# Optimization experiments

Hardware: AMD Instinct MI355X
Metric: run time of the kernel (lower is better)

## Reference

```python
import jax, jax.numpy as jnp
import numpy as np

N_NODES = 100000
N_EDGES = 1600000
D_IN = 128
D_OUT = 5


def setup_inputs() -> dict:
    key = jax.random.key(0)
    k1, k2, k3, k4, k5 = jax.random.split(key, 5)
    x = jax.random.normal(k1, (N_NODES, D_IN), dtype=jnp.float32)
    edge_index = jax.random.randint(k2, (2, N_EDGES), 0, N_NODES, dtype=jnp.int64)
    scale = 1.0 / np.sqrt(D_IN)
    W_l = jax.random.normal(k3, (D_OUT, D_IN), dtype=jnp.float32) * scale
    b_l = jax.random.normal(k4, (D_OUT,), dtype=jnp.float32) * scale
    W_r = jax.random.normal(k5, (D_OUT, D_IN), dtype=jnp.float32) * scale
    return {"x": x, "edge_index": edge_index, "W_l": W_l, "b_l": b_l, "W_r": W_r}


def reference(x, edge_index, W_l, b_l, W_r):
    # PyG SAGEConv with aggr='mean', root_weight=True:
    # out_i = mean_{j: (j->i) in E} x_j @ W_l^T + b_l + x_i @ W_r^T
    n = x.shape[0]
    src = edge_index[0]
    dst = edge_index[1]
    msgs = x[src]  # [E, D_in] gather (irregular access)
    agg_sum = jax.ops.segment_sum(msgs, dst, num_segments=n)  # [N, D_in]
    deg = jax.ops.segment_sum(jnp.ones(src.shape, dtype=x.dtype), dst, num_segments=n)
    agg_mean = agg_sum / jnp.maximum(deg, 1.0)[:, None]  # zero-degree nodes -> 0
    out = agg_mean @ W_l.T + b_l + x @ W_r.T  # [N, D_out]
    return out
```

## Files before the change

kernel.cpp:

```cpp
#include <hip/hip_runtime.h>
#include <hip/hip_bf16.h>


#define N_NODES 100000
#define N_EDGES 1600000
#define D_IN 128

#define HL_STRIDE 8
#define N_PAD 100352

#define B_NODES 196
#define N_BUCKETS 512
#define CAP 3840

#define SC_EPB 16384
#define SC_GRID ((N_EDGES + SC_EPB - 1) / SC_EPB)
#define SC_CHUNKS (SC_EPB / 1024)

#define NPG 8
#define PROJ_NPB (16 * NPG)
#define PROJ_BLOCKS ((N_NODES + PROJ_NPB - 1) / PROJ_NPB)
#define FUSED_GRID (SC_GRID + PROJ_BLOCKS)

#define FXS 262144.0f
#define FXB 16777216u
#define FXBF 16777216.0f
#define INV_FXS (1.0f / 262144.0f)

typedef unsigned long long u64;
typedef unsigned int u32;

__global__ __launch_bounds__(256, 4) void proj_scatter_kernel(
    const float* __restrict__ x,
    const float* __restrict__ Wl,
    const float* __restrict__ Wr,
    float* __restrict__ hl,
    float* __restrict__ hr,
    const int* __restrict__ ei,
    u32* __restrict__ sorted,
    int* __restrict__ cursor)
{
    const int tid = threadIdx.x;

    if (blockIdx.x < SC_GRID) {
        __shared__ int hist[N_BUCKETS];
        __shared__ int basepos[N_BUCKETS];

        for (int i = tid; i < N_BUCKETS; i += 256) hist[i] = 0;
        __syncthreads();

        const int e0 = blockIdx.x * SC_EPB;

#pragma unroll
        for (int c = 0; c < SC_CHUNKS; ++c) {
            int e = e0 + (c << 10) + (tid << 2);
            if (e < N_EDGES) {
                int4 d4 = *(const int4*)(ei + N_EDGES + e);
                atomicAdd(&hist[(unsigned)d4.x / 196u], 1);
                atomicAdd(&hist[(unsigned)d4.y / 196u], 1);
                atomicAdd(&hist[(unsigned)d4.z / 196u], 1);
                atomicAdd(&hist[(unsigned)d4.w / 196u], 1);
            }
        }
        __syncthreads();

        for (int b = tid; b < N_BUCKETS; b += 256) {
            int c = hist[b];
            if (c > 0) basepos[b] = atomicAdd(&cursor[b], c);
        }
        __syncthreads();

        for (int i = tid; i < N_BUCKETS; i += 256) hist[i] = 0;
        __syncthreads();

#pragma unroll
        for (int c = 0; c < SC_CHUNKS; ++c) {
            int e = e0 + (c << 10) + (tid << 2);
            if (e < N_EDGES) {
                int4 s4 = *(const int4*)(ei + e);
                int4 d4 = *(const int4*)(ei + N_EDGES + e);
                int sv[4] = { s4.x, s4.y, s4.z, s4.w };
                int dv[4] = { d4.x, d4.y, d4.z, d4.w };
#pragma unroll
                for (int q = 0; q < 4; ++q) {
                    unsigned b = (unsigned)dv[q] / 196u;
                    unsigned r = (unsigned)dv[q] - b * 196u;
                    int slot = atomicAdd(&hist[b], 1);
                    sorted[(size_t)b * CAP + basepos[b] + slot] =
                        (r << 17) | (unsigned)sv[q];
                }
            }
        }
    } else {
        const int pblk = blockIdx.x - SC_GRID;
        const int g = tid >> 4;
        const int k = tid & 15;

        float4 wv[10][2];
#pragma unroll
        for (int o = 0; o < 10; ++o) {
            const float* w = (o < 5 ? Wl + o * D_IN : Wr + (o - 5) * D_IN) + k * 8;
            wv[o][0] = ((const float4*)w)[0];
            wv[o][1] = ((const float4*)w)[1];
        }

        const int node0 = pblk * PROJ_NPB + g * NPG;

#pragma unroll
        for (int it = 0; it < NPG; ++it) {
            const int node = min(node0 + it, N_NODES - 1);

            const float4* xr = (const float4*)(x + (size_t)node * D_IN + k * 8);
            float4 x0 = xr[0];
            float4 x1 = xr[1];

            float s[10];
#pragma unroll
            for (int o = 0; o < 10; ++o) {
                s[o] = x0.x * wv[o][0].x + x0.y * wv[o][0].y
                     + x0.z * wv[o][0].z + x0.w * wv[o][0].w
                     + x1.x * wv[o][1].x + x1.y * wv[o][1].y
                     + x1.z * wv[o][1].z + x1.w * wv[o][1].w;
            }

#pragma unroll
            for (int o = 0; o < 10; ++o) {
                s[o] += __shfl_xor(s[o], 8, 64);
                s[o] += __shfl_xor(s[o], 4, 64);
                s[o] += __shfl_xor(s[o], 2, 64);
                s[o] += __shfl_xor(s[o], 1, 64);
            }

            if (k == 0) {
                float* pl = hl + (size_t)node * HL_STRIDE;
                *(float4*)pl = make_float4(s[0], s[1], s[2], s[3]);
                pl[4] = s[4];
                float* pr = hr + (size_t)node * HL_STRIDE;
                *(float4*)pr = make_float4(s[5], s[6], s[7], s[8]);
                pr[4] = s[9];
            }
        }
    }
}

__global__ __launch_bounds__(512) void agg_kernel(
    const u32* __restrict__ sorted,
    const int* __restrict__ cursor,
    const float* __restrict__ hl,
    const float* __restrict__ hr,
    const float* __restrict__ bias,
    float* __restrict__ out)
{
    __shared__ u64 acc[B_NODES * 3];

    const int b   = blockIdx.x;
    const int tid = threadIdx.x;

    for (int i = tid; i < B_NODES * 3; i += 512) acc[i] = 0ull;
    __syncthreads();

    const int cnt = cursor[b];
    const u32* sp = sorted + (size_t)b * CAP;
    const int nvec = cnt >> 2;

#define EMIT(hh, ee, rr)                                                     \
    {                                                                        \
        u32 f0 = __float2uint_rn(fmaf((hh).x, FXS, FXBF));                   \
        u32 f1 = __float2uint_rn(fmaf((hh).y, FXS, FXBF));                   \
        u32 f2 = __float2uint_rn(fmaf((hh).z, FXS, FXBF));                   \
        u32 f3 = __float2uint_rn(fmaf((hh).w, FXS, FXBF));                   \
        u32 f4 = __float2uint_rn(fmaf((ee),   FXS, FXBF));                   \
        u64* a = acc + (rr) * 3;                                             \
        atomicAdd(&a[0], ((u64)f1 << 32) | f0);                              \
        atomicAdd(&a[1], ((u64)f3 << 32) | f2);                              \
        atomicAdd(&a[2], ((u64)f4 << 32) | 1u);                              \
    }

    for (int it = tid; it < nvec; it += 512) {
        uint4 v = ((const uint4*)sp)[it];
        int s0 = (int)(v.x & 0x1FFFFu), r0 = (int)(v.x >> 17);
        int s1 = (int)(v.y & 0x1FFFFu), r1 = (int)(v.y >> 17);
        int s2 = (int)(v.z & 0x1FFFFu), r2 = (int)(v.z >> 17);
        int s3 = (int)(v.w & 0x1FFFFu), r3 = (int)(v.w >> 17);

        const float* p0 = hl + (size_t)s0 * HL_STRIDE;
        const float* p1 = hl + (size_t)s1 * HL_STRIDE;
        const float* p2 = hl + (size_t)s2 * HL_STRIDE;
        const float* p3 = hl + (size_t)s3 * HL_STRIDE;
        float4 h0 = *(const float4*)p0; float e0 = p0[4];
        float4 h1 = *(const float4*)p1; float e1 = p1[4];
        float4 h2 = *(const float4*)p2; float e2 = p2[4];
        float4 h3 = *(const float4*)p3; float e3 = p3[4];

        EMIT(h0, e0, r0) EMIT(h1, e1, r1) EMIT(h2, e2, r2) EMIT(h3, e3, r3)
    }
    for (int i = (nvec << 2) + tid; i < cnt; i += 512) {
        u32 v = sp[i];
        int src = (int)(v & 0x1FFFFu);
        int r   = (int)(v >> 17);
        const float* p = hl + (size_t)src * HL_STRIDE;
        float4 h = *(const float4*)p;
        float  e = p[4];
        EMIT(h, e, r)
    }
#undef EMIT
    __syncthreads();

    const int nodebase = b * B_NODES;
    for (int n = tid; n < B_NODES; n += 512) {
        int node = nodebase + n;
        if (node >= N_NODES) continue;
        u64 w0 = acc[n * 3 + 0];
        u64 w1 = acc[n * 3 + 1];
        u64 w2 = acc[n * 3 + 2];
        u32 deg = (u32)(w2 & 0xFFFFFFFFu);
        u32 db  = deg * FXB;
        int i0 = (int)((u32)(w0 & 0xFFFFFFFFu) - db);
        int i1 = (int)((u32)(w0 >> 32)         - db);
        int i2 = (int)((u32)(w1 & 0xFFFFFFFFu) - db);
        int i3 = (int)((u32)(w1 >> 32)         - db);
        int i4 = (int)((u32)(w2 >> 32)         - db);

        float rec = INV_FXS / fmaxf((float)deg, 1.0f);
        const float* h = hr + (size_t)node * HL_STRIDE;
        float* o = out + (size_t)node * 5;
        o[0] = (float)i0 * rec + bias[0] + h[0];
        o[1] = (float)i1 * rec + bias[1] + h[1];
        o[2] = (float)i2 * rec + bias[2] + h[2];
        o[3] = (float)i3 * rec + bias[3] + h[3];
        o[4] = (float)i4 * rec + bias[4] + h[4];
    }
}

extern "C" void kernel_launch(void* const* d_in, const int* in_sizes, int n_in,
                              void* d_out, int out_size, void* d_ws, size_t ws_size,
                              hipStream_t stream) {
    const float* x    = (const float*)d_in[0];
    const int*   ei   = (const int*)d_in[1];
    const float* Wl   = (const float*)d_in[2];
    const float* bl   = (const float*)d_in[3];
    const float* Wr   = (const float*)d_in[4];
    float*       out  = (float*)d_out;

    float* hl     = (float*)d_ws;
    float* hr     = hl + (size_t)N_PAD * HL_STRIDE;
    u32*   sorted = (u32*)(hr + (size_t)N_PAD * HL_STRIDE);
    int*   cursor = (int*)(sorted + (size_t)N_BUCKETS * CAP);

    hipMemsetAsync(cursor, 0, N_BUCKETS * sizeof(int), stream);

    proj_scatter_kernel<<<FUSED_GRID, 256, 0, stream>>>(
        x, Wl, Wr, hl, hr, ei, sorted, cursor);

    agg_kernel<<<N_BUCKETS, 512, 0, stream>>>(sorted, cursor, hl, hr, bl, out);
}
```

Baseline: 140.3 us.

## Keep edges in registers across scatter passes and widen aggregation gather to eight

Result: no change. 140.0 us (-0.2%).

```diff
diff --git a/kernel.cpp b/kernel.cpp
--- a/kernel.cpp
+++ b/kernel.cpp
@@ -13,9 +13,9 @@
 #define N_BUCKETS 512
 #define CAP 3840
 
-#define SC_EPB 16384
+#define SC_EPB 4096
 #define SC_GRID ((N_EDGES + SC_EPB - 1) / SC_EPB)
-#define SC_CHUNKS (SC_EPB / 1024)
+#define SC_EPT 16
 
 #define NPG 8
 #define PROJ_NPB (16 * NPG)
@@ -49,17 +49,31 @@
         for (int i = tid; i < N_BUCKETS; i += 256) hist[i] = 0;
         __syncthreads();
 
-        const int e0 = blockIdx.x * SC_EPB;
-
-#pragma unroll
-        for (int c = 0; c < SC_CHUNKS; ++c) {
-            int e = e0 + (c << 10) + (tid << 2);
-            if (e < N_EDGES) {
+        const int eb = blockIdx.x * SC_EPB;
+
+        int sv[SC_EPT], dv[SC_EPT], slot[SC_EPT];
+        bool vld[4];
+
+#pragma unroll
+        for (int c = 0; c < 4; ++c) {
+            int e = eb + (c << 10) + (tid << 2);
+            vld[c] = (e < N_EDGES);
+            if (vld[c]) {
+                int4 s4 = *(const int4*)(ei + e);
                 int4 d4 = *(const int4*)(ei + N_EDGES + e);
-                atomicAdd(&hist[(unsigned)d4.x / 196u], 1);
-                atomicAdd(&hist[(unsigned)d4.y / 196u], 1);
-                atomicAdd(&hist[(unsigned)d4.z / 196u], 1);
-                atomicAdd(&hist[(unsigned)d4.w / 196u], 1);
+                sv[c*4+0]=s4.x; sv[c*4+1]=s4.y; sv[c*4+2]=s4.z; sv[c*4+3]=s4.w;
+                dv[c*4+0]=d4.x; dv[c*4+1]=d4.y; dv[c*4+2]=d4.z; dv[c*4+3]=d4.w;
+            }
+        }
+
+#pragma unroll
+        for (int c = 0; c < 4; ++c) {
+            if (vld[c]) {
+#pragma unroll
+                for (int q = 0; q < 4; ++q) {
+                    unsigned b = (unsigned)dv[c*4+q] / 196u;
+                    slot[c*4+q] = atomicAdd(&hist[b], 1);
+                }
             }
         }
         __syncthreads();
@@ -70,24 +84,15 @@
         }
         __syncthreads();
 
-        for (int i = tid; i < N_BUCKETS; i += 256) hist[i] = 0;
-        __syncthreads();
-
-#pragma unroll
-        for (int c = 0; c < SC_CHUNKS; ++c) {
-            int e = e0 + (c << 10) + (tid << 2);
-            if (e < N_EDGES) {
-                int4 s4 = *(const int4*)(ei + e);
-                int4 d4 = *(const int4*)(ei + N_EDGES + e);
-                int sv[4] = { s4.x, s4.y, s4.z, s4.w };
-                int dv[4] = { d4.x, d4.y, d4.z, d4.w };
+#pragma unroll
+        for (int c = 0; c < 4; ++c) {
+            if (vld[c]) {
 #pragma unroll
                 for (int q = 0; q < 4; ++q) {
-                    unsigned b = (unsigned)dv[q] / 196u;
-                    unsigned r = (unsigned)dv[q] - b * 196u;
-                    int slot = atomicAdd(&hist[b], 1);
-                    sorted[(size_t)b * CAP + basepos[b] + slot] =
-                        (r << 17) | (unsigned)sv[q];
+                    unsigned b = (unsigned)dv[c*4+q] / 196u;
+                    unsigned r = (unsigned)dv[c*4+q] - b * 196u;
+                    sorted[(size_t)b * CAP + basepos[b] + slot[c*4+q]] =
+                        (r << 17) | (unsigned)sv[c*4+q];
                 }
             }
         }
@@ -161,7 +166,6 @@
 
     const int cnt = cursor[b];
     const u32* sp = sorted + (size_t)b * CAP;
-    const int nvec = cnt >> 2;
 
 #define EMIT(hh, ee, rr)                                                     \
     {                                                                        \
@@ -176,32 +180,33 @@
         atomicAdd(&a[2], ((u64)f4 << 32) | 1u);                              \
     }
 
-    for (int it = tid; it < nvec; it += 512) {
-        uint4 v = ((const uint4*)sp)[it];
-        int s0 = (int)(v.x & 0x1FFFFu), r0 = (int)(v.x >> 17);
-        int s1 = (int)(v.y & 0x1FFFFu), r1 = (int)(v.y >> 17);
-        int s2 = (int)(v.z & 0x1FFFFu), r2 = (int)(v.z >> 17);
-        int s3 = (int)(v.w & 0x1FFFFu), r3 = (int)(v.w >> 17);
-
-        const float* p0 = hl + (size_t)s0 * HL_STRIDE;
-        const float* p1 = hl + (size_t)s1 * HL_STRIDE;
-        const float* p2 = hl + (size_t)s2 * HL_STRIDE;
-        const float* p3 = hl + (size_t)s3 * HL_STRIDE;
-        float4 h0 = *(const float4*)p0; float e0 = p0[4];
-        float4 h1 = *(const float4*)p1; float e1 = p1[4];
-        float4 h2 = *(const float4*)p2; float e2 = p2[4];
-        float4 h3 = *(const float4*)p3; float e3 = p3[4];
-
-        EMIT(h0, e0, r0) EMIT(h1, e1, r1) EMIT(h2, e2, r2) EMIT(h3, e3, r3)
-    }
-    for (int i = (nvec << 2) + tid; i < cnt; i += 512) {
+    const int noct = cnt >> 3;
+    for (int it = tid; it < noct; it += 512) {
+        const uint4* sp4 = (const uint4*)sp;
+        uint4 va = sp4[it * 2];
+        uint4 vb = sp4[it * 2 + 1];
+        u32 rec[8] = { va.x, va.y, va.z, va.w, vb.x, vb.y, vb.z, vb.w };
+
+        const float* p[8];
+#pragma unroll
+        for (int q = 0; q < 8; ++q)
+            p[q] = hl + (size_t)(rec[q] & 0x1FFFFu) * HL_STRIDE;
+
+        float4 h[8]; float e[8];
+#pragma unroll
+        for (int q = 0; q < 8; ++q) { h[q] = *(const float4*)p[q]; e[q] = p[q][4]; }
+
+#pragma unroll
+        for (int q = 0; q < 8; ++q) EMIT(h[q], e[q], (int)(rec[q] >> 17))
+    }
+    for (int i = (noct << 3) + tid; i < cnt; i += 512) {
         u32 v = sp[i];
         int src = (int)(v & 0x1FFFFu);
         int r   = (int)(v >> 17);
-        const float* p = hl + (size_t)src * HL_STRIDE;
-        float4 h = *(const float4*)p;
-        float  e = p[4];
-        EMIT(h, e, r)
+        const float* pp = hl + (size_t)src * HL_STRIDE;
+        float4 hh = *(const float4*)pp;
+        float  ee = pp[4];
+        EMIT(hh, ee, r)
     }
 #undef EMIT
     __syncthreads();
```
